# Optimization experiments

Hardware: AMD Instinct MI355X
Metric: run time of the kernel (lower is better)

## Reference

```python
import jax, jax.numpy as jnp
import numpy as np


def setup_inputs() -> dict:
    key = jax.random.key(0)
    k1, k2, k3 = jax.random.split(key, 3)
    B, H, S, D = 2, 8, 4096, 64
    queries = jax.random.normal(k1, (B, H, S, D), dtype=jnp.float32)
    keys = jax.random.normal(k2, (B, H, S, D), dtype=jnp.float32)
    values = jax.random.normal(k3, (B, H, S, D), dtype=jnp.float32)
    mask = jnp.zeros((1, 1, S, S), dtype=jnp.float32)
    return {"queries": queries, "keys": keys, "values": values, "d_k": D, "mask": mask}


def reference(queries, keys, values, d_k, mask):
    # scores: [B, H, Sq, Sk]
    scale = 1.0 / jnp.sqrt(jnp.asarray(d_k, dtype=queries.dtype))
    scores = jnp.einsum("bhqd,bhkd->bhqk", queries, keys) * scale
    scores = scores + (-1e9) * mask  # additive mask, broadcasts over B, H
    weights = jax.nn.softmax(scores, axis=-1)
    return jnp.einsum("bhqk,bhkd->bhqd", weights, values)
```

## Files before the change

kernel.cpp:

```cpp
#include <hip/hip_runtime.h>

#define S_LEN 4096
#define DHEAD 64
#define BK    64
#define NT    (S_LEN / BK)
#define NBH   16
#define KPAD  72
#define BQ    128
#define TILE_HALFS (BK * DHEAD)
#define WS_KV_HALFS ((size_t)NBH * NT * TILE_HALFS)

typedef __fp16   pk16x2 __attribute__((ext_vector_type(2)));
typedef _Float16 half4v __attribute__((ext_vector_type(4)));
typedef _Float16 half8  __attribute__((ext_vector_type(8)));
typedef float    f32x4  __attribute__((ext_vector_type(4)));
typedef float    f32x16 __attribute__((ext_vector_type(16)));
typedef unsigned uint2v __attribute__((ext_vector_type(2)));

#define MFMA32(a, b, c) __builtin_amdgcn_mfma_f32_32x32x16_f16(a, b, c, 0, 0, 0)

__device__ __forceinline__ void gl_lds16(const _Float16* g, _Float16* l) {
    __builtin_amdgcn_global_load_lds(
        (const __attribute__((address_space(1))) unsigned int*)g,
        (__attribute__((address_space(3))) unsigned int*)l, 16, 0, 0);
}

__device__ __forceinline__ unsigned pk2u(float a, float b) {
    union { pk16x2 p; unsigned u; } x;
    x.p = __builtin_amdgcn_cvt_pkrtz(a, b);
    return x.u;
}

__device__ __forceinline__ uint2v pls(unsigned x, unsigned y) {
    return __builtin_amdgcn_permlane32_swap(x, y, false, false);
}
__device__ __forceinline__ float xmax32(float v) {
    uint2v r = pls(__float_as_uint(v), __float_as_uint(v));
    return fmaxf(__uint_as_float(r.x), __uint_as_float(r.y));
}

__global__ void mask_flag_kernel(const float4* __restrict__ mask, int* __restrict__ flag) {
    const long stride = 2048L * 256;
    long i = (long)blockIdx.x * 256 + threadIdx.x;
    int nz = 0;
    #pragma unroll
    for (int it = 0; it < 8; ++it) {
        float4 a = mask[i + it * stride];
        nz |= (a.x != 0.f) | (a.y != 0.f) | (a.z != 0.f) | (a.w != 0.f);
    }
    if (__any(nz)) {
        if ((threadIdx.x & 63) == 0) atomicOr(flag, 1);
    }
}

__global__ void conv_kernel(const float* __restrict__ Kg, const float* __restrict__ Vg,
                            const float* __restrict__ mask,
                            _Float16* __restrict__ wsK, _Float16* __restrict__ wsV,
                            int* __restrict__ flag) {
    const int tid  = threadIdx.x;
    const int tile = blockIdx.x;
    __shared__ __align__(16) _Float16 T[64][64];

    if (blockIdx.y == 0) {
        const float* Ksrc = Kg + (long)tile * TILE_HALFS;
        _Float16*    dst  = wsK + (long)tile * TILE_HALFS;
        #pragma unroll
        for (int it = 0; it < 2; ++it) {
            int m = tid + it * 256;
            int r = m >> 3, c = m & 7;
            const float4* s4 = (const float4*)(Ksrc + r * DHEAD + ((c ^ (r & 7)) << 3));
            float4 a = s4[0], b = s4[1];
            union { pk16x2 p[4]; half8 h; } u;
            u.p[0] = __builtin_amdgcn_cvt_pkrtz(a.x, a.y);
            u.p[1] = __builtin_amdgcn_cvt_pkrtz(a.z, a.w);
            u.p[2] = __builtin_amdgcn_cvt_pkrtz(b.x, b.y);
            u.p[3] = __builtin_amdgcn_cvt_pkrtz(b.z, b.w);
            *(half8*)(dst + m * 8) = u.h;
        }
    } else if (blockIdx.y == 1) {
        const float* Vsrc = Vg + (long)tile * TILE_HALFS;
        const int r  = tid >> 2;
        const int d0 = (tid & 3) << 4;
        const float4* s4 = (const float4*)(Vsrc + r * DHEAD + d0);
        float vv[16];
        *(float4*)&vv[0]  = s4[0];
        *(float4*)&vv[4]  = s4[1];
        *(float4*)&vv[8]  = s4[2];
        *(float4*)&vv[12] = s4[3];
        #pragma unroll
        for (int j = 0; j < 16; j += 2) {
            pk16x2 p = __builtin_amdgcn_cvt_pkrtz(vv[j], vv[j + 1]);
            T[d0 + j][r]     = *((_Float16*)&p);
            T[d0 + j + 1][r] = *((_Float16*)&p + 1);
        }
        __syncthreads();
        _Float16* dst = wsV + (long)tile * TILE_HALFS;
        #pragma unroll
        for (int it = 0; it < 2; ++it) {
            int m = tid + it * 256;
            int d = m >> 3, c = m & 7;
            *(half8*)(dst + m * 8) = *(const half8*)&T[d][(c ^ (d & 7)) << 3];
        }
    } else {
        const float4* m4 = (const float4*)mask;
        const long stride = 1024L * 256;
        long i = (long)blockIdx.x * 256 + tid;
        int nz = 0;
        #pragma unroll
        for (int it = 0; it < 16; ++it) {
            float4 a = m4[i + it * stride];
            nz |= (a.x != 0.f) | (a.y != 0.f) | (a.z != 0.f) | (a.w != 0.f);
        }
        if (__any(nz)) {
            if ((tid & 63) == 0) atomicOr(flag, 1);
        }
    }
}

__global__ __launch_bounds__(512, 4) void attn32x_kernel(
    const float* __restrict__ Q, const _Float16* __restrict__ KW,
    const _Float16* __restrict__ VW, const int* __restrict__ dkp,
    const float* __restrict__ mask, const int* __restrict__ maskflag,
    float* __restrict__ O)
{
    const int bid = blockIdx.x;
    const int L   = (bid & 7) * 64 + (bid >> 3);
    const int bh  = L >> 5;
    const int qt  = L & 31;

    const int tid  = threadIdx.x;
    const int hf   = tid >> 8;
    const int t    = tid & 255;
    const int w    = (tid >> 6) & 3;
    const int lane = tid & 63;
    const int l31  = lane & 31;
    const int h    = lane >> 5;
    const int cx   = lane & 7;

    const int HT  = NT / 2;
    const int kt0 = hf * HT;

    const long gbase = (long)bh * S_LEN * DHEAD;
    const float* Qh = Q + gbase;
    const _Float16* gk = KW + (long)bh * (NT * TILE_HALFS);
    const _Float16* gv = VW + (long)bh * (NT * TILE_HALFS);

    const int q0 = qt * 128 + w * 32;
    const float csq  = rsqrtf((float)dkp[0]) * 1.44269504088896f;
    const float mfac = -1e9f * 1.44269504088896f;
    const bool use_mask = (maskflag[0] != 0);

    __shared__ __align__(16) _Float16 KT[2][2][TILE_HALFS];
    __shared__ __align__(16) _Float16 VT[2][2][TILE_HALFS];

    half8 qf[4];
    #pragma unroll
    for (int ks = 0; ks < 4; ++ks) {
        const float4* src = (const float4*)(Qh + (long)(q0 + l31) * DHEAD + ks * 16 + h * 8);
        float4 a = src[0], b = src[1];
        union { unsigned u[4]; half8 h8; } u;
        u.u[0] = pk2u(a.x * csq, a.y * csq);
        u.u[1] = pk2u(a.z * csq, a.w * csq);
        u.u[2] = pk2u(b.x * csq, b.y * csq);
        u.u[3] = pk2u(b.z * csq, b.w * csq);
        qf[ks] = u.h8;
    }

    half8 vones;
    #pragma unroll
    for (int j = 0; j < 8; ++j) vones[j] = (_Float16)1.0f;

    auto stage = [&](int kt, int bb) {
        const _Float16* k8 = gk + (long)kt * TILE_HALFS + t * 8;
        const _Float16* v8 = gv + (long)kt * TILE_HALFS + t * 8;
        gl_lds16(k8,        &KT[hf][bb][t * 8]);
        gl_lds16(k8 + 2048, &KT[hf][bb][2048 + t * 8]);
        gl_lds16(v8,        &VT[hf][bb][t * 8]);
        gl_lds16(v8 + 2048, &VT[hf][bb][2048 + t * 8]);
    };

    f32x16 o0 = {0.f,0.f,0.f,0.f,0.f,0.f,0.f,0.f,0.f,0.f,0.f,0.f,0.f,0.f,0.f,0.f};
    f32x16 o1 = o0;
    f32x16 ol = o0;
    float m_i = -INFINITY;

    stage(kt0, 0);
    __syncthreads();

    for (int lt = 0; lt < HT; ++lt) {
        const int kt = kt0 + lt;
        const int b  = lt & 1;
        if (lt + 1 < HT) stage(kt + 1, b ^ 1);

        f32x16 s0 = {0.f,0.f,0.f,0.f,0.f,0.f,0.f,0.f,0.f,0.f,0.f,0.f,0.f,0.f,0.f,0.f};
        f32x16 s1 = s0;
        __builtin_amdgcn_s_setprio(1);
        #pragma unroll
        for (int ks = 0; ks < 4; ++ks) {
            const int off = (((2 * ks + h) ^ cx) << 3);
            half8 a0 = *(const half8*)&KT[hf][b][(l31 << 6) + off];
            half8 a1 = *(const half8*)&KT[hf][b][2048 + (l31 << 6) + off];
            s0 = MFMA32(a0, qf[ks], s0);
            s1 = MFMA32(a1, qf[ks], s1);
        }
        __builtin_amdgcn_s_setprio(0);

        if (use_mask) {
            const float* mrow = mask + (long)(q0 + l31) * S_LEN + kt * BK;
            #pragma unroll
            for (int r = 0; r < 16; ++r) {
                const int k = (r & 3) + ((r >> 2) << 3) + (h << 2);
                s0[r] += mfac * mrow[k];
                s1[r] += mfac * mrow[32 + k];
            }
        }

        {
            float tt[8];
            #pragma unroll
            for (int i = 0; i < 8; ++i)
                tt[i] = fmaxf(fmaxf(s0[2*i], s0[2*i+1]), fmaxf(s1[2*i], s1[2*i+1]));
            float mx = fmaxf(fmaxf(fmaxf(tt[0], tt[1]), fmaxf(tt[2], tt[3])),
                             fmaxf(fmaxf(tt[4], tt[5]), fmaxf(tt[6], tt[7])));
            mx = xmax32(mx);
            const bool need = __any(mx > m_i + 8.0f);
            const float mnew = need ? fmaxf(m_i, mx) : m_i;
            #pragma unroll
            for (int r = 0; r < 16; ++r) {
                s0[r] = __builtin_amdgcn_exp2f(s0[r] - mnew);
                s1[r] = __builtin_amdgcn_exp2f(s1[r] - mnew);
            }
            if (need) {
                const float alpha = __builtin_amdgcn_exp2f(m_i - mnew);
                #pragma unroll
                for (int r = 0; r < 16; ++r) {
                    const int qr = (r & 3) + ((r >> 2) << 3) + (h << 2);
                    float a_r = __shfl(alpha, qr, 64);
                    o0[r] *= a_r; o1[r] *= a_r; ol[r] *= a_r;
                }
                m_i = mnew;
            }
        }

        unsigned wp[16];
        #pragma unroll
        for (int d = 0; d < 8; ++d) {
            wp[d]     = pk2u(s0[2*d], s0[2*d+1]);
            wp[8 + d] = pk2u(s1[2*d], s1[2*d+1]);
        }

        __builtin_amdgcn_s_setprio(1);
        #pragma unroll
        for (int si = 0; si < 4; ++si) {
            const int bs = (si >> 1) * 8 + (si & 1) * 4;
            uint2v r0 = pls(wp[bs + 0], wp[bs + 2]);
            uint2v r1 = pls(wp[bs + 1], wp[bs + 3]);
            union { unsigned u[4]; half8 h8; } pa;
            pa.u[0] = r0.x; pa.u[1] = r1.x; pa.u[2] = r0.y; pa.u[3] = r1.y;
            const int off = (((2 * si + h) ^ cx) << 3);
            half8 v0 = *(const half8*)&VT[hf][b][(l31 << 6) + off];
            half8 v1 = *(const half8*)&VT[hf][b][2048 + (l31 << 6) + off];
            o0 = MFMA32(pa.h8, v0, o0);
            o1 = MFMA32(pa.h8, v1, o1);
            ol = MFMA32(pa.h8, vones, ol);
        }
        __builtin_amdgcn_s_setprio(0);

        if (lt + 1 < HT) __syncthreads();
    }

    const int  rr  = (l31 & 3) + ((l31 >> 3) << 2);
    const bool own = (((l31 >> 2) & 1) == h);
    float lv = ol[0];
    #pragma unroll
    for (int r = 1; r < 16; ++r) lv = (rr == r) ? ol[r] : lv;

    float*  comb = (float*)&KT[0][0][0];
    float2* mlA  = (float2*)&VT[0][0][0];
    float2* mlB  = mlA + 128;

    __syncthreads();
    if (hf == 1) {
        #pragma unroll
        for (int r = 0; r < 16; ++r) {
            const int qr = (r & 3) + ((r >> 2) << 3) + (h << 2);
            comb[w * 2048 + qr * 64 + l31]      = o0[r];
            comb[w * 2048 + qr * 64 + 32 + l31] = o1[r];
        }
        if (own) mlB[w * 32 + l31] = make_float2(m_i, lv);
    } else {
        if (own) mlA[w * 32 + l31] = make_float2(m_i, lv);
    }
    __syncthreads();

    if (hf == 0) {
        float* dst = O + gbase;
        #pragma unroll
        for (int r = 0; r < 16; ++r) {
            const int qr = (r & 3) + ((r >> 2) << 3) + (h << 2);
            const float2 ml1 = mlA[w * 32 + qr];
            const float2 ml2 = mlB[w * 32 + qr];
            const float m   = fmaxf(ml1.x, ml2.x);
            const float a1  = __builtin_amdgcn_exp2f(ml1.x - m);
            const float a2  = __builtin_amdgcn_exp2f(ml2.x - m);
            const float inv = __builtin_amdgcn_rcpf(ml1.y * a1 + ml2.y * a2);
            const float p0  = comb[w * 2048 + qr * 64 + l31];
            const float p1  = comb[w * 2048 + qr * 64 + 32 + l31];
            const long row = (long)(q0 + qr) * DHEAD;
            dst[row + l31]      = (o0[r] * a1 + p0 * a2) * inv;
            dst[row + 32 + l31] = (o1[r] * a1 + p1 * a2) * inv;
        }
    }
}

__global__ __launch_bounds__(256, 2) void attn_kernel_fb(
    const float* __restrict__ Q, const float* __restrict__ K,
    const float* __restrict__ V, const int* __restrict__ dk,
    const float* __restrict__ mask, const int* __restrict__ maskflag,
    float* __restrict__ O)
{
    const int qt   = blockIdx.x;
    const int bh   = blockIdx.y;
    const int tid  = threadIdx.x;
    const int wave = tid >> 6;
    const int lane = tid & 63;
    const int l15  = lane & 15;
    const int quad = lane >> 4;

    const long base = (long)bh * S_LEN * DHEAD;
    const float* Qh = Q + base;
    const float* Kh = K + base;
    const float* Vh = V + base;
    float*       Oh = O + base;

    const int q0 = qt * BQ + wave * 32;
    const float csq  = rsqrtf((float)dk[0]) * 1.44269504088896f;
    const float mfac = -1e9f * 1.44269504088896f;
    const bool use_mask = (maskflag[0] != 0);

    __shared__ __align__(16) _Float16 Kt[2][BK][KPAD];
    __shared__ __align__(16) _Float16 Vt[2][DHEAD * KPAD];
    __shared__ __align__(16) _Float16 Pw[4][32][KPAD];

    half8 qf[2][2];
    #pragma unroll
    for (int f = 0; f < 2; ++f) {
        #pragma unroll
        for (int kc = 0; kc < 2; ++kc) {
            const float4* src = (const float4*)(Qh + (long)(q0 + f*16 + l15) * DHEAD + kc*32 + quad*8);
            float4 a = src[0], b = src[1];
            union { pk16x2 p[4]; half8 h; } u;
            u.p[0] = __builtin_amdgcn_cvt_pkrtz(a.x*csq, a.y*csq);
            u.p[1] = __builtin_amdgcn_cvt_pkrtz(a.z*csq, a.w*csq);
            u.p[2] = __builtin_amdgcn_cvt_pkrtz(b.x*csq, b.y*csq);
            u.p[3] = __builtin_amdgcn_cvt_pkrtz(b.z*csq, b.w*csq);
            qf[f][kc] = u.h;
        }
    }

    const int kr  = tid >> 2;
    const int ks  = tid & 3;
    const int vrp = tid >> 3;
    const int vdq = tid & 7;
    const float* Kb = Kh + (long)kr * DHEAD + ks * 16;
    const float* Vb = Vh + (long)(2 * vrp) * DHEAD + vdq * 8;
    const int vcol = (((vrp >> 2) ^ vdq) << 3) + ((2 * vrp) & 7);
    const int vd0  = vdq * 8;

    float4 kf[4], vf[4];
    auto load_tile = [&](int kt) {
        const float4* kp  = (const float4*)(Kb + (long)kt * BK * DHEAD);
        kf[0] = kp[0]; kf[1] = kp[1]; kf[2] = kp[2]; kf[3] = kp[3];
        const float4* vp0 = (const float4*)(Vb + (long)kt * BK * DHEAD);
        const float4* vp1 = (const float4*)(Vb + (long)kt * BK * DHEAD + DHEAD);
        vf[0] = vp0[0]; vf[1] = vp0[1]; vf[2] = vp1[0]; vf[3] = vp1[1];
    };
    auto store_tile = [&](int b) {
        union { pk16x2 p[4]; half8 h; } u0, u1;
        u0.p[0] = __builtin_amdgcn_cvt_pkrtz(kf[0].x, kf[0].y);
        u0.p[1] = __builtin_amdgcn_cvt_pkrtz(kf[0].z, kf[0].w);
        u0.p[2] = __builtin_amdgcn_cvt_pkrtz(kf[1].x, kf[1].y);
        u0.p[3] = __builtin_amdgcn_cvt_pkrtz(kf[1].z, kf[1].w);
        u1.p[0] = __builtin_amdgcn_cvt_pkrtz(kf[2].x, kf[2].y);
        u1.p[1] = __builtin_amdgcn_cvt_pkrtz(kf[2].z, kf[2].w);
        u1.p[2] = __builtin_amdgcn_cvt_pkrtz(kf[3].x, kf[3].y);
        u1.p[3] = __builtin_amdgcn_cvt_pkrtz(kf[3].z, kf[3].w);
        *(half8*)&Kt[b][kr][ks*16]     = u0.h;
        *(half8*)&Kt[b][kr][ks*16 + 8] = u1.h;
        _Float16* vt = &Vt[b][0];
        *(pk16x2*)&vt[(vd0+0)*KPAD + vcol] = __builtin_amdgcn_cvt_pkrtz(vf[0].x, vf[2].x);
        *(pk16x2*)&vt[(vd0+1)*KPAD + vcol] = __builtin_amdgcn_cvt_pkrtz(vf[0].y, vf[2].y);
        *(pk16x2*)&vt[(vd0+2)*KPAD + vcol] = __builtin_amdgcn_cvt_pkrtz(vf[0].z, vf[2].z);
        *(pk16x2*)&vt[(vd0+3)*KPAD + vcol] = __builtin_amdgcn_cvt_pkrtz(vf[0].w, vf[2].w);
        *(pk16x2*)&vt[(vd0+4)*KPAD + vcol] = __builtin_amdgcn_cvt_pkrtz(vf[1].x, vf[3].x);
        *(pk16x2*)&vt[(vd0+5)*KPAD + vcol] = __builtin_amdgcn_cvt_pkrtz(vf[1].y, vf[3].y);
        *(pk16x2*)&vt[(vd0+6)*KPAD + vcol] = __builtin_amdgcn_cvt_pkrtz(vf[1].z, vf[3].z);
        *(pk16x2*)&vt[(vd0+7)*KPAD + vcol] = __builtin_amdgcn_cvt_pkrtz(vf[1].w, vf[3].w);
    };

    f32x4 o[2][4];
    #pragma unroll
    for (int f = 0; f < 2; ++f)
        #pragma unroll
        for (int dt = 0; dt < 4; ++dt) o[f][dt] = (f32x4){0.f, 0.f, 0.f, 0.f};
    float m_i[2] = {-INFINITY, -INFINITY};
    float l_i[2] = {0.0f, 0.0f};

    load_tile(0);
    store_tile(0);
    __syncthreads();

    for (int kt = 0; kt < NT; ++kt) {
        const int b = kt & 1;
        if (kt + 1 < NT) load_tile(kt + 1);

        f32x4 st[2][4];
        #pragma unroll
        for (int f = 0; f < 2; ++f)
            #pragma unroll
            for (int nt = 0; nt < 4; ++nt) st[f][nt] = (f32x4){0.f,0.f,0.f,0.f};
        #pragma unroll
        for (int nt = 0; nt < 4; ++nt) {
            #pragma unroll
            for (int kc = 0; kc < 2; ++kc) {
                half8 af = *(const half8*)&Kt[b][nt*16 + l15][kc*32 + quad*8];
                st[0][nt] = __builtin_amdgcn_mfma_f32_16x16x32_f16(af, qf[0][kc], st[0][nt], 0, 0, 0);
                st[1][nt] = __builtin_amdgcn_mfma_f32_16x16x32_f16(af, qf[1][kc], st[1][nt], 0, 0, 0);
            }
        }

        if (use_mask) {
            #pragma unroll
            for (int f = 0; f < 2; ++f) {
                const long mrow = (long)(q0 + f*16 + l15) * S_LEN + kt*BK;
                #pragma unroll
                for (int nt = 0; nt < 4; ++nt)
                    #pragma unroll
                    for (int r = 0; r < 4; ++r)
                        st[f][nt][r] += mfac * mask[mrow + nt*16 + quad*4 + r];
            }
        }

        float alpha[2];
        #pragma unroll
        for (int f = 0; f < 2; ++f) {
            float mx = fmaxf(fmaxf(fmaxf(st[f][0][0], st[f][0][1]), fmaxf(st[f][0][2], st[f][0][3])),
                             fmaxf(fmaxf(st[f][1][0], st[f][1][1]), fmaxf(st[f][1][2], st[f][1][3])));
            float mx2 = fmaxf(fmaxf(fmaxf(st[f][2][0], st[f][2][1]), fmaxf(st[f][2][2], st[f][2][3])),
                              fmaxf(fmaxf(st[f][3][0], st[f][3][1]), fmaxf(st[f][3][2], st[f][3][3])));
            mx = fmaxf(mx, mx2);
            mx = fmaxf(mx, __shfl_xor(mx, 16, 64));
            mx = fmaxf(mx, __shfl_xor(mx, 32, 64));
            float mnew = fmaxf(m_i[f], mx);
            float rsum = 0.0f;
            #pragma unroll
            for (int nt = 0; nt < 4; ++nt) {
                #pragma unroll
                for (int r = 0; r < 4; ++r) {
                    float p = __builtin_amdgcn_exp2f(st[f][nt][r] - mnew);
                    st[f][nt][r] = p;
                    rsum += p;
                }
            }
            rsum += __shfl_xor(rsum, 16, 64);
            rsum += __shfl_xor(rsum, 32, 64);
            alpha[f] = __builtin_amdgcn_exp2f(m_i[f] - mnew);
            l_i[f] = alpha[f] * l_i[f] + rsum;
            m_i[f] = mnew;
        }

        #pragma unroll
        for (int f = 0; f < 2; ++f)
            #pragma unroll
            for (int r = 0; r < 4; ++r) {
                float a_r = __shfl(alpha[f], quad*4 + r, 64);
                #pragma unroll
                for (int dt = 0; dt < 4; ++dt) o[f][dt][r] *= a_r;
            }

        #pragma unroll
        for (int f = 0; f < 2; ++f)
            #pragma unroll
            for (int nt = 0; nt < 4; ++nt) {
                union { pk16x2 p[2]; half4v h; } up;
                up.p[0] = __builtin_amdgcn_cvt_pkrtz(st[f][nt][0], st[f][nt][1]);
                up.p[1] = __builtin_amdgcn_cvt_pkrtz(st[f][nt][2], st[f][nt][3]);
                *(half4v*)&Pw[wave][f*16 + l15][nt*16 + quad*4] = up.h;
            }

        #pragma unroll
        for (int kc2 = 0; kc2 < 2; ++kc2) {
            half8 pa0 = *(const half8*)&Pw[wave][l15][kc2*32 + quad*8];
            half8 pa1 = *(const half8*)&Pw[wave][16 + l15][kc2*32 + quad*8];
            #pragma unroll
            for (int dt = 0; dt < 4; ++dt) {
                const int row = dt*16 + l15;
                const int pb  = (4*kc2 + quad) ^ (row >> 3);
                half8 vb = *(const half8*)&Vt[b][row*KPAD + pb*8];
                o[0][dt] = __builtin_amdgcn_mfma_f32_16x16x32_f16(pa0, vb, o[0][dt], 0, 0, 0);
                o[1][dt] = __builtin_amdgcn_mfma_f32_16x16x32_f16(pa1, vb, o[1][dt], 0, 0, 0);
            }
        }

        if (kt + 1 < NT) {
            store_tile((kt + 1) & 1);
            __syncthreads();
        }
    }

    #pragma unroll
    for (int f = 0; f < 2; ++f) {
        #pragma unroll
        for (int r = 0; r < 4; ++r) {
            float lq = __shfl(l_i[f], quad*4 + r, 64);
            float linv = __builtin_amdgcn_rcpf(lq);
            const long row = (long)(q0 + f*16 + quad*4 + r) * DHEAD;
            #pragma unroll
            for (int dt = 0; dt < 4; ++dt)
                Oh[row + dt*16 + l15] = o[f][dt][r] * linv;
        }
    }
}

extern "C" void kernel_launch(void* const* d_in, const int* in_sizes, int n_in,
                              void* d_out, int out_size, void* d_ws, size_t ws_size,
                              hipStream_t stream) {
    const float* Q    = (const float*)d_in[0];
    const float* K    = (const float*)d_in[1];
    const float* V    = (const float*)d_in[2];
    const int*   dk   = (const int*)d_in[3];
    const float* mask = (const float*)d_in[4];
    float* out = (float*)d_out;
    int* ctrl = (int*)d_ws;

    (void)hipMemsetAsync(ctrl, 0, 256, stream);

    const size_t CTRL      = 256;
    const size_t KV_BYTES  = 2 * WS_KV_HALFS * sizeof(_Float16);
    const size_t NEED_BASE = CTRL + KV_BYTES;

    if (ws_size >= NEED_BASE) {
        _Float16* wsK = (_Float16*)((char*)d_ws + CTRL);
        _Float16* wsV = wsK + WS_KV_HALFS;
        conv_kernel<<<dim3(NBH * NT, 3), 256, 0, stream>>>(K, V, mask, wsK, wsV, ctrl);
        attn32x_kernel<<<512, 512, 0, stream>>>(Q, wsK, wsV, dk, mask, ctrl, out);
    } else {
        mask_flag_kernel<<<2048, 256, 0, stream>>>((const float4*)mask, ctrl);
        dim3 grid(S_LEN / BQ, NBH);
        attn_kernel_fb<<<grid, 256, 0, stream>>>(Q, K, V, dk, mask, ctrl, out);
    }
}
```

Measured before the change: 274.6 us.

## Fuse K/V fp16 conversion into attention kernel and track row sums with shuffles

```diff
diff --git a/kernel.cpp b/kernel.cpp
--- a/kernel.cpp
+++ b/kernel.cpp
@@ -8,7 +8,6 @@
 #define KPAD  72
 #define BQ    128
 #define TILE_HALFS (BK * DHEAD)
-#define WS_KV_HALFS ((size_t)NBH * NT * TILE_HALFS)
 
 typedef __fp16   pk16x2 __attribute__((ext_vector_type(2)));
 typedef _Float16 half4v __attribute__((ext_vector_type(4)));
@@ -19,12 +18,6 @@
 
 #define MFMA32(a, b, c) __builtin_amdgcn_mfma_f32_32x32x16_f16(a, b, c, 0, 0, 0)
 
-__device__ __forceinline__ void gl_lds16(const _Float16* g, _Float16* l) {
-    __builtin_amdgcn_global_load_lds(
-        (const __attribute__((address_space(1))) unsigned int*)g,
-        (__attribute__((address_space(3))) unsigned int*)l, 16, 0, 0);
-}
-
 __device__ __forceinline__ unsigned pk2u(float a, float b) {
     union { pk16x2 p; unsigned u; } x;
     x.p = __builtin_amdgcn_cvt_pkrtz(a, b);
@@ -37,6 +30,10 @@
 __device__ __forceinline__ float xmax32(float v) {
     uint2v r = pls(__float_as_uint(v), __float_as_uint(v));
     return fmaxf(__uint_as_float(r.x), __uint_as_float(r.y));
+}
+__device__ __forceinline__ float xadd32(float v) {
+    uint2v r = pls(__float_as_uint(v), __float_as_uint(v));
+    return __uint_as_float(r.x) + __uint_as_float(r.y);
 }
 
 __global__ void mask_flag_kernel(const float4* __restrict__ mask, int* __restrict__ flag) {
@@ -53,73 +50,9 @@
     }
 }
 
-__global__ void conv_kernel(const float* __restrict__ Kg, const float* __restrict__ Vg,
-                            const float* __restrict__ mask,
-                            _Float16* __restrict__ wsK, _Float16* __restrict__ wsV,
-                            int* __restrict__ flag) {
-    const int tid  = threadIdx.x;
-    const int tile = blockIdx.x;
-    __shared__ __align__(16) _Float16 T[64][64];
-
-    if (blockIdx.y == 0) {
-        const float* Ksrc = Kg + (long)tile * TILE_HALFS;
-        _Float16*    dst  = wsK + (long)tile * TILE_HALFS;
-        #pragma unroll
-        for (int it = 0; it < 2; ++it) {
-            int m = tid + it * 256;
-            int r = m >> 3, c = m & 7;
-            const float4* s4 = (const float4*)(Ksrc + r * DHEAD + ((c ^ (r & 7)) << 3));
-            float4 a = s4[0], b = s4[1];
-            union { pk16x2 p[4]; half8 h; } u;
-            u.p[0] = __builtin_amdgcn_cvt_pkrtz(a.x, a.y);
-            u.p[1] = __builtin_amdgcn_cvt_pkrtz(a.z, a.w);
-            u.p[2] = __builtin_amdgcn_cvt_pkrtz(b.x, b.y);
-            u.p[3] = __builtin_amdgcn_cvt_pkrtz(b.z, b.w);
-            *(half8*)(dst + m * 8) = u.h;
-        }
-    } else if (blockIdx.y == 1) {
-        const float* Vsrc = Vg + (long)tile * TILE_HALFS;
-        const int r  = tid >> 2;
-        const int d0 = (tid & 3) << 4;
-        const float4* s4 = (const float4*)(Vsrc + r * DHEAD + d0);
-        float vv[16];
-        *(float4*)&vv[0]  = s4[0];
-        *(float4*)&vv[4]  = s4[1];
-        *(float4*)&vv[8]  = s4[2];
-        *(float4*)&vv[12] = s4[3];
-        #pragma unroll
-        for (int j = 0; j < 16; j += 2) {
-            pk16x2 p = __builtin_amdgcn_cvt_pkrtz(vv[j], vv[j + 1]);
-            T[d0 + j][r]     = *((_Float16*)&p);
-            T[d0 + j + 1][r] = *((_Float16*)&p + 1);
-        }
-        __syncthreads();
-        _Float16* dst = wsV + (long)tile * TILE_HALFS;
-        #pragma unroll
-        for (int it = 0; it < 2; ++it) {
-            int m = tid + it * 256;
-            int d = m >> 3, c = m & 7;
-            *(half8*)(dst + m * 8) = *(const half8*)&T[d][(c ^ (d & 7)) << 3];
-        }
-    } else {
-        const float4* m4 = (const float4*)mask;
-        const long stride = 1024L * 256;
-        long i = (long)blockIdx.x * 256 + tid;
-        int nz = 0;
-        #pragma unroll
-        for (int it = 0; it < 16; ++it) {
-            float4 a = m4[i + it * stride];
-            nz |= (a.x != 0.f) | (a.y != 0.f) | (a.z != 0.f) | (a.w != 0.f);
-        }
-        if (__any(nz)) {
-            if ((tid & 63) == 0) atomicOr(flag, 1);
-        }
-    }
-}
-
-__global__ __launch_bounds__(512, 4) void attn32x_kernel(
-    const float* __restrict__ Q, const _Float16* __restrict__ KW,
-    const _Float16* __restrict__ VW, const int* __restrict__ dkp,
+__global__ __launch_bounds__(512, 4) void attn32f_kernel(
+    const float* __restrict__ Q, const float* __restrict__ K,
+    const float* __restrict__ V, const int* __restrict__ dkp,
     const float* __restrict__ mask, const int* __restrict__ maskflag,
     float* __restrict__ O)
 {
@@ -136,14 +69,15 @@
     const int l31  = lane & 31;
     const int h    = lane >> 5;
     const int cx   = lane & 7;
+    const int vkey = (l31 ^ (l31 >> 3)) & 7;
 
     const int HT  = NT / 2;
     const int kt0 = hf * HT;
 
     const long gbase = (long)bh * S_LEN * DHEAD;
     const float* Qh = Q + gbase;
-    const _Float16* gk = KW + (long)bh * (NT * TILE_HALFS);
-    const _Float16* gv = VW + (long)bh * (NT * TILE_HALFS);
+    const float* Kh = K + gbase;
+    const float* Vh = V + gbase;
 
     const int q0 = qt * 128 + w * 32;
     const float csq  = rsqrtf((float)dkp[0]) * 1.44269504088896f;
@@ -166,31 +100,64 @@
         qf[ks] = u.h8;
     }
 
-    half8 vones;
-    #pragma unroll
-    for (int j = 0; j < 8; ++j) vones[j] = (_Float16)1.0f;
-
-    auto stage = [&](int kt, int bb) {
-        const _Float16* k8 = gk + (long)kt * TILE_HALFS + t * 8;
-        const _Float16* v8 = gv + (long)kt * TILE_HALFS + t * 8;
-        gl_lds16(k8,        &KT[hf][bb][t * 8]);
-        gl_lds16(k8 + 2048, &KT[hf][bb][2048 + t * 8]);
-        gl_lds16(v8,        &VT[hf][bb][t * 8]);
-        gl_lds16(v8 + 2048, &VT[hf][bb][2048 + t * 8]);
+    const int kr  = t >> 2;
+    const int ks4 = t & 3;
+    const int vrp = t >> 3;
+    const int vdq = t & 7;
+    const float* Kb = Kh + (long)kr * DHEAD + ks4 * 16;
+    const float* Vb = Vh + (long)(2 * vrp) * DHEAD + vdq * 8;
+    const int kcol0 = (((2 * ks4)     ^ (kr & 7)) << 3);
+    const int kcol1 = (((2 * ks4 + 1) ^ (kr & 7)) << 3);
+    const int vd0   = vdq * 8;
+    const int voct  = vrp >> 2;
+    const int vlow  = (2 * vrp) & 7;
+
+    float4 kf[4], vf[4];
+    auto load_tile = [&](int kt) {
+        const float4* kp  = (const float4*)(Kb + (long)kt * TILE_HALFS);
+        kf[0] = kp[0]; kf[1] = kp[1]; kf[2] = kp[2]; kf[3] = kp[3];
+        const float4* vp0 = (const float4*)(Vb + (long)kt * TILE_HALFS);
+        const float4* vp1 = (const float4*)(Vb + (long)kt * TILE_HALFS + DHEAD);
+        vf[0] = vp0[0]; vf[1] = vp0[1]; vf[2] = vp1[0]; vf[3] = vp1[1];
+    };
+    auto store_tile = [&](int bb) {
+        union { unsigned u[4]; half8 h8; } u0, u1;
+        u0.u[0] = pk2u(kf[0].x, kf[0].y);
+        u0.u[1] = pk2u(kf[0].z, kf[0].w);
+        u0.u[2] = pk2u(kf[1].x, kf[1].y);
+        u0.u[3] = pk2u(kf[1].z, kf[1].w);
+        u1.u[0] = pk2u(kf[2].x, kf[2].y);
+        u1.u[1] = pk2u(kf[2].z, kf[2].w);
+        u1.u[2] = pk2u(kf[3].x, kf[3].y);
+        u1.u[3] = pk2u(kf[3].z, kf[3].w);
+        *(half8*)&KT[hf][bb][kr * 64 + kcol0] = u0.h8;
+        *(half8*)&KT[hf][bb][kr * 64 + kcol1] = u1.h8;
+        _Float16* vt = &VT[hf][bb][0];
+        #define VCOL(j) ((((voct ^ (j) ^ vdq) & 7) << 3) + vlow)
+        *(pk16x2*)&vt[(vd0 + 0) * 64 + VCOL(0)] = __builtin_amdgcn_cvt_pkrtz(vf[0].x, vf[2].x);
+        *(pk16x2*)&vt[(vd0 + 1) * 64 + VCOL(1)] = __builtin_amdgcn_cvt_pkrtz(vf[0].y, vf[2].y);
+        *(pk16x2*)&vt[(vd0 + 2) * 64 + VCOL(2)] = __builtin_amdgcn_cvt_pkrtz(vf[0].z, vf[2].z);
+        *(pk16x2*)&vt[(vd0 + 3) * 64 + VCOL(3)] = __builtin_amdgcn_cvt_pkrtz(vf[0].w, vf[2].w);
+        *(pk16x2*)&vt[(vd0 + 4) * 64 + VCOL(4)] = __builtin_amdgcn_cvt_pkrtz(vf[1].x, vf[3].x);
+        *(pk16x2*)&vt[(vd0 + 5) * 64 + VCOL(5)] = __builtin_amdgcn_cvt_pkrtz(vf[1].y, vf[3].y);
+        *(pk16x2*)&vt[(vd0 + 6) * 64 + VCOL(6)] = __builtin_amdgcn_cvt_pkrtz(vf[1].z, vf[3].z);
+        *(pk16x2*)&vt[(vd0 + 7) * 64 + VCOL(7)] = __builtin_amdgcn_cvt_pkrtz(vf[1].w, vf[3].w);
+        #undef VCOL
     };
 
     f32x16 o0 = {0.f,0.f,0.f,0.f,0.f,0.f,0.f,0.f,0.f,0.f,0.f,0.f,0.f,0.f,0.f,0.f};
     f32x16 o1 = o0;
-    f32x16 ol = o0;
     float m_i = -INFINITY;
-
-    stage(kt0, 0);
+    float l_i = 0.0f;
+
+    load_tile(kt0);
+    store_tile(0);
     __syncthreads();
 
     for (int lt = 0; lt < HT; ++lt) {
         const int kt = kt0 + lt;
         const int b  = lt & 1;
-        if (lt + 1 < HT) stage(kt + 1, b ^ 1);
+        if (lt + 1 < HT) load_tile(kt + 1);
 
         f32x16 s0 = {0.f,0.f,0.f,0.f,0.f,0.f,0.f,0.f,0.f,0.f,0.f,0.f,0.f,0.f,0.f,0.f};
         f32x16 s1 = s0;
@@ -225,20 +192,27 @@
             mx = xmax32(mx);
             const bool need = __any(mx > m_i + 8.0f);
             const float mnew = need ? fmaxf(m_i, mx) : m_i;
+            float ra = 0.f, rb = 0.f;
             #pragma unroll
             for (int r = 0; r < 16; ++r) {
-                s0[r] = __builtin_amdgcn_exp2f(s0[r] - mnew);
-                s1[r] = __builtin_amdgcn_exp2f(s1[r] - mnew);
-            }
+                float p0 = __builtin_amdgcn_exp2f(s0[r] - mnew);
+                float p1 = __builtin_amdgcn_exp2f(s1[r] - mnew);
+                s0[r] = p0; s1[r] = p1;
+                ra += p0; rb += p1;
+            }
+            float rsum = xadd32(ra + rb);
             if (need) {
                 const float alpha = __builtin_amdgcn_exp2f(m_i - mnew);
                 #pragma unroll
                 for (int r = 0; r < 16; ++r) {
                     const int qr = (r & 3) + ((r >> 2) << 3) + (h << 2);
                     float a_r = __shfl(alpha, qr, 64);
-                    o0[r] *= a_r; o1[r] *= a_r; ol[r] *= a_r;
+                    o0[r] *= a_r; o1[r] *= a_r;
                 }
+                l_i = alpha * l_i + rsum;
                 m_i = mnew;
+            } else {
+                l_i += rsum;
             }
         }
 
@@ -257,23 +231,19 @@
             uint2v r1 = pls(wp[bs + 1], wp[bs + 3]);
             union { unsigned u[4]; half8 h8; } pa;
             pa.u[0] = r0.x; pa.u[1] = r1.x; pa.u[2] = r0.y; pa.u[3] = r1.y;
-            const int off = (((2 * si + h) ^ cx) << 3);
-            half8 v0 = *(const half8*)&VT[hf][b][(l31 << 6) + off];
-            half8 v1 = *(const half8*)&VT[hf][b][2048 + (l31 << 6) + off];
+            const int voff = (((2 * si + h) ^ vkey) << 3);
+            half8 v0 = *(const half8*)&VT[hf][b][(l31 << 6) + voff];
+            half8 v1 = *(const half8*)&VT[hf][b][2048 + (l31 << 6) + (voff ^ 32)];
             o0 = MFMA32(pa.h8, v0, o0);
             o1 = MFMA32(pa.h8, v1, o1);
-            ol = MFMA32(pa.h8, vones, ol);
         }
         __builtin_amdgcn_s_setprio(0);
 
-        if (lt + 1 < HT) __syncthreads();
-    }
-
-    const int  rr  = (l31 & 3) + ((l31 >> 3) << 2);
-    const bool own = (((l31 >> 2) & 1) == h);
-    float lv = ol[0];
-    #pragma unroll
-    for (int r = 1; r < 16; ++r) lv = (rr == r) ? ol[r] : lv;
+        if (lt + 1 < HT) {
+            store_tile(b ^ 1);
+            __syncthreads();
+        }
+    }
 
     float*  comb = (float*)&KT[0][0][0];
     float2* mlA  = (float2*)&VT[0][0][0];
@@ -287,9 +257,9 @@
             comb[w * 2048 + qr * 64 + l31]      = o0[r];
             comb[w * 2048 + qr * 64 + 32 + l31] = o1[r];
         }
-        if (own) mlB[w * 32 + l31] = make_float2(m_i, lv);
+        if (h == 0) mlB[w * 32 + l31] = make_float2(m_i, l_i);
     } else {
-        if (own) mlA[w * 32 + l31] = make_float2(m_i, lv);
+        if (h == 0) mlA[w * 32 + l31] = make_float2(m_i, l_i);
     }
     __syncthreads();
 
@@ -531,22 +501,15 @@
     const int*   dk   = (const int*)d_in[3];
     const float* mask = (const float*)d_in[4];
     float* out = (float*)d_out;
-    int* ctrl = (int*)d_ws;
-
-    (void)hipMemsetAsync(ctrl, 0, 256, stream);
-
-    const size_t CTRL      = 256;
-    const size_t KV_BYTES  = 2 * WS_KV_HALFS * sizeof(_Float16);
-    const size_t NEED_BASE = CTRL + KV_BYTES;
-
-    if (ws_size >= NEED_BASE) {
-        _Float16* wsK = (_Float16*)((char*)d_ws + CTRL);
-        _Float16* wsV = wsK + WS_KV_HALFS;
-        conv_kernel<<<dim3(NBH * NT, 3), 256, 0, stream>>>(K, V, mask, wsK, wsV, ctrl);
-        attn32x_kernel<<<512, 512, 0, stream>>>(Q, wsK, wsV, dk, mask, ctrl, out);
+    int* flag = (int*)d_ws;
+
+    (void)hipMemsetAsync(flag, 0, sizeof(int), stream);
+    mask_flag_kernel<<<2048, 256, 0, stream>>>((const float4*)mask, flag);
+
+    if (ws_size >= 256) {
+        attn32f_kernel<<<512, 512, 0, stream>>>(Q, K, V, dk, mask, flag, out);
     } else {
-        mask_flag_kernel<<<2048, 256, 0, stream>>>((const float4*)mask, ctrl);
         dim3 grid(S_LEN / BQ, NBH);
-        attn_kernel_fb<<<grid, 256, 0, stream>>>(Q, K, V, dk, mask, ctrl, out);
-    }
-}
+        attn_kernel_fb<<<grid, 256, 0, stream>>>(Q, K, V, dk, mask, flag, out);
+    }
+}
```

Measured after the change: 606.6 us. 121% more time.
